# Performance work log

Hardware: AMD Instinct MI355X
Metric: run time of the kernel (lower is better)

Reference implementation:

```python
import jax, jax.numpy as jnp
import numpy as np

B, SQ, SK, D = 8, 2048, 2048, 256

def setup_inputs() -> dict:
    key = jax.random.key(0)
    ks = jax.random.split(key, 8)
    x1 = jax.random.normal(ks[0], (B, SQ, D), dtype=jnp.float32)
    x2 = jax.random.normal(ks[1], (B, SK, D), dtype=jnp.float32)
    x3 = jax.random.normal(ks[2], (B, SK, D), dtype=jnp.float32)  # unused by the original forward (value=x3 is dead)
    mask = jax.random.bernoulli(ks[3], 0.8, (B, SK))
    scale = 0.02
    Wq = jax.random.normal(ks[4], (D, D), dtype=jnp.float32) * scale
    Wk = jax.random.normal(ks[5], (D, D), dtype=jnp.float32) * scale
    Wv = jax.random.normal(ks[6], (D, D), dtype=jnp.float32) * scale
    bq = jnp.zeros((D,), jnp.float32)
    bk = jnp.zeros((D,), jnp.float32)
    bv = jnp.zeros((D,), jnp.float32)
    return {"x1": x1, "x2": x2, "x3": x3, "Wq": Wq, "Wk": Wk, "Wv": Wv,
            "bq": bq, "bk": bk, "bv": bv, "mask": mask}

def reference(x1, x2, x3, Wq, Wk, Wv, bq, bk, bv, mask):
    d = x1.shape[-1]
    inv_sqrt_d = 1.0 / jnp.sqrt(jnp.asarray(d, x1.dtype))
    # Projections (single-head MHA with query scaling, as in torch MHA internals)
    q = (x1 @ Wq + bq) * inv_sqrt_d          # [B, SQ, D]
    k = x2 @ Wk + bk                          # [B, SK, D]
    v = x2 @ Wv + bv                          # forward_value(key): value projected from key input
    # Raw scores
    qk = jnp.einsum('bqd,bkd->bqk', q, k)     # [B, SQ, SK]
    # Mask-derived per-column rescale: qk /= (mask.size(0)/mask.sum(-2))**0.5
    m = mask.astype(qk.dtype)                 # [B, SK]
    col_count = jnp.sum(m, axis=0, keepdims=True)           # [1, SK]
    factor = jnp.sqrt(jnp.asarray(mask.shape[0], qk.dtype) / col_count)  # [1, SK]
    qk = qk / factor                          # broadcast over [B, SQ, SK]; div-by-inf -> 0 where column count is 0
    attn = jax.nn.softmax(qk, axis=-1)
    # dropout is identity in eval / p=0
    out = jnp.einsum('bqk,bkd->bqd', attn, v)  # [B, SQ, D]
    return out
```

## Files before the change

### kernel.cpp

```cpp
#include <hip/hip_runtime.h>
#include <hip/hip_bf16.h>
#include <math.h>

#define B_  8
#define SQ_ 2048
#define SK_ 2048
#define D_  256
#define NSPLIT 4
#define KEYS_PER_SPLIT (SK_ / NSPLIT)
#define NT (KEYS_PER_SPLIT / 32)

typedef __attribute__((ext_vector_type(8))) short bf16x8;
typedef __attribute__((ext_vector_type(4))) float f32x4;
typedef __attribute__((ext_vector_type(4))) unsigned short u16x4;
typedef __attribute__((ext_vector_type(8))) _Float16 f16x8;
typedef __attribute__((ext_vector_type(4))) _Float16 f16x4;
typedef __attribute__((ext_vector_type(4))) unsigned int u32x4;

static __device__ __forceinline__ unsigned short f2bf(float f) {
    unsigned int u = __builtin_bit_cast(unsigned int, f);
    u += 0x7FFFu + ((u >> 16) & 1u);
    return (unsigned short)(u >> 16);
}

static __device__ __forceinline__ void gld_lds16(const unsigned short* g, unsigned short* l) {
    __builtin_amdgcn_global_load_lds(
        (const __attribute__((address_space(1))) unsigned int*)g,
        (__attribute__((address_space(3))) unsigned int*)l, 16, 0, 0);
}

__global__ void prep_kernel(const float* __restrict__ Wq, const float* __restrict__ Wk,
                            const float* __restrict__ Wv, const int* __restrict__ mask,
                            unsigned short* __restrict__ wP, float* __restrict__ r) {
    int bid = blockIdx.x, tid = threadIdx.x;
    if (bid < 96) {
        int p = bid >> 5, c = (bid >> 2) & 7, it = bid & 3;
        const float* W = (p == 0 ? Wq : (p == 1 ? Wk : Wv));
        int chunk = it * 256 + tid;
        int nt = chunk >> 6, lane = chunk & 63;
        int l15 = lane & 15, quad = lane >> 4;
        int n = nt * 16 + l15;
        unsigned short* dst = wP + (size_t)(((p * 8 + c) * 16 + nt) * 1024 + lane * 8);
#pragma unroll
        for (int j = 0; j < 8; j++)
            dst[j] = f2bf(W[(size_t)(c * 32 + quad * 8 + j) * D_ + n]);
    } else {
        int s = (bid - 96) * 256 + tid;
        float c = 0.f;
#pragma unroll
        for (int b = 0; b < B_; b++) c += (mask[b * SK_ + s] != 0) ? 1.f : 0.f;
        r[s] = sqrtf(c * 0.125f);
    }
}

__global__ __launch_bounds__(256) void proj_kernel(
    const float* __restrict__ x1, const float* __restrict__ x2,
    const float* __restrict__ bq, const float* __restrict__ bk, const float* __restrict__ bv,
    const unsigned short* __restrict__ wP, const float* __restrict__ r,
    unsigned short* __restrict__ qb, unsigned short* __restrict__ kP,
    unsigned short* __restrict__ vP)
{
    __shared__ unsigned short sbuf[18432];
    const int tid = threadIdx.x;
    const int wv = tid >> 6, lane = tid & 63, l15 = lane & 15, quad = lane >> 4;
    const int mt = blockIdx.x, b = blockIdx.y, p = blockIdx.z;
    const int s0w = mt * 64 + wv * 16;

    const float* x = (p == 0 ? x1 : x2) + ((size_t)b * SQ_ + s0w + l15) * D_;
    const unsigned short* wbase = wP + (size_t)(p * 8) * 16 * 1024;
    const float* bias = (p == 0 ? bq : (p == 1 ? bk : bv));

    float4 xa[8], xb[8];
#pragma unroll
    for (int c = 0; c < 8; c++) {
        xa[c] = *(const float4*)(x + c * 32 + quad * 8);
        xb[c] = *(const float4*)(x + c * 32 + quad * 8 + 4);
    }
    bf16x8 af[8];
#pragma unroll
    for (int c = 0; c < 8; c++) {
        bf16x8 t;
        t[0] = (short)f2bf(xa[c].x); t[1] = (short)f2bf(xa[c].y);
        t[2] = (short)f2bf(xa[c].z); t[3] = (short)f2bf(xa[c].w);
        t[4] = (short)f2bf(xb[c].x); t[5] = (short)f2bf(xb[c].y);
        t[6] = (short)f2bf(xb[c].z); t[7] = (short)f2bf(xb[c].w);
        af[c] = t;
    }

    float bb[16];
#pragma unroll
    for (int nt = 0; nt < 16; nt++) bb[nt] = bias[nt * 16 + l15];

    f32x4 acc[16];
#pragma unroll
    for (int n = 0; n < 16; n++) acc[n] = (f32x4){0.f, 0.f, 0.f, 0.f};

#pragma unroll
    for (int c = 0; c < 8; c++) {
        const unsigned short* wc = wbase + (size_t)c * 16 * 1024 + lane * 8;
#pragma unroll
        for (int nt = 0; nt < 16; nt++) {
            bf16x8 wf = *(const bf16x8*)(wc + nt * 1024);
            acc[nt] = __builtin_amdgcn_mfma_f32_16x16x32_bf16(af[c], wf, acc[nt], 0, 0, 0);
        }
    }

    if (p == 2) {
#pragma unroll
        for (int nt = 0; nt < 16; nt++) {
            int d = nt * 16 + l15;
            u16x4 u;
#pragma unroll
            for (int g = 0; g < 4; g++) u[g] = f2bf(acc[nt][g] + bb[nt]);
            *(u16x4*)(sbuf + (size_t)d * 72 + wv * 16 + quad * 4) = u;
        }
        __syncthreads();
#pragma unroll
        for (int it = 0; it < 8; it++) {
            int chunk = it * 256 + tid;
            int tt = chunk >> 10, n = (chunk >> 6) & 15, ln = chunk & 63;
            bf16x8 v = *(const bf16x8*)(sbuf + (size_t)(n * 16 + (ln & 15)) * 72 + tt * 32 + (ln >> 4) * 8);
            *(bf16x8*)(vP + (((size_t)(b * 64 + mt * 2 + tt) * 16 + n) * 512) + ln * 8) = v;
        }
    } else if (p == 0) {
        float rv = 0.0625f;
        unsigned short* my = sbuf + wv * 2176;
#pragma unroll
        for (int h = 0; h < 2; h++) {
#pragma unroll
            for (int nt8 = 0; nt8 < 8; nt8++) {
                int nt = h * 8 + nt8;
#pragma unroll
                for (int g = 0; g < 4; g++) {
                    float v = (acc[nt][g] + bb[nt]) * rv;
                    my[(quad * 4 + g) * 136 + nt8 * 16 + l15] = f2bf(v);
                }
            }
            asm volatile("s_waitcnt lgkmcnt(0)" ::: "memory");
#pragma unroll
            for (int i2 = 0; i2 < 4; i2++) {
                int row = i2 * 4 + quad;
                bf16x8 v = *(const bf16x8*)(my + row * 136 + l15 * 8);
                *(bf16x8*)(qb + ((size_t)(b * SQ_ + s0w + row)) * D_ + h * 128 + l15 * 8) = v;
            }
        }
    } else {
        const int t = mt * 2 + (wv >> 1), hfrag = wv & 1;
        float rv[4];
#pragma unroll
        for (int g = 0; g < 4; g++) rv[g] = r[s0w + quad * 4 + g];
        unsigned short* my = sbuf + wv * 2176;
#pragma unroll
        for (int hp = 0; hp < 2; hp++) {
#pragma unroll
            for (int nt8 = 0; nt8 < 8; nt8++) {
                int nt = hp * 8 + nt8;
#pragma unroll
                for (int g = 0; g < 4; g++) {
                    float v = (acc[nt][g] + bb[nt]) * rv[g];
                    my[(quad * 4 + g) * 136 + nt8 * 16 + l15] = f2bf(v);
                }
            }
            asm volatile("s_waitcnt lgkmcnt(0)" ::: "memory");
#pragma unroll
            for (int cc = 0; cc < 4; cc++) {
                bf16x8 v = *(const bf16x8*)(my + (size_t)l15 * 136 + cc * 32 + quad * 8);
                *(bf16x8*)(kP + ((((size_t)(b * 64 + t) * 2 + hfrag) * 8 + hp * 4 + cc) * 512) + lane * 8) = v;
            }
        }
    }
}

__global__ __launch_bounds__(256, 2) void flash_kernel(
    const unsigned short* __restrict__ qb, const unsigned short* __restrict__ kP,
    const unsigned short* __restrict__ vP, _Float16* __restrict__ Op,
    float* __restrict__ lp)
{
    __shared__ unsigned short Ks[2][16 * 512];
    __shared__ unsigned short Vs[2][16 * 512];
    const int tid = threadIdx.x;
    const int wv = tid >> 6, lane = tid & 63, l15 = lane & 15, quad = lane >> 4;
    const int bid = blockIdx.x;
    const int g = bid & 31, q = bid >> 5;
    const int b = g >> 2, sp = g & 3;
    const int q0 = q * 128 + wv * 32;

    const unsigned short* kpb = kP + (size_t)(b * 64 + sp * 16) * 8192;
    const unsigned short* vpb = vP + (size_t)(b * 64 + sp * 16) * 8192;

    const int c0 = tid * 8;

#pragma unroll
    for (int i = 0; i < 4; i++)
        gld_lds16(kpb + (size_t)i * 2048 + c0, &Ks[0][i * 2048 + wv * 512]);
#pragma unroll
    for (int i = 0; i < 4; i++)
        gld_lds16(vpb + (size_t)i * 2048 + c0, &Vs[0][i * 2048 + wv * 512]);

    bf16x8 qf[2][8];
#pragma unroll
    for (int mt = 0; mt < 2; mt++) {
        const unsigned short* qrow = qb + ((size_t)(b * SQ_ + q0 + mt * 16 + l15)) * D_;
#pragma unroll
        for (int c = 0; c < 8; c++)
            qf[mt][c] = *(const bf16x8*)(qrow + c * 32 + quad * 8);
    }

    f32x4 o[2][16];
#pragma unroll
    for (int mt = 0; mt < 2; mt++)
#pragma unroll
        for (int n = 0; n < 16; n++) o[mt][n] = (f32x4){0.f, 0.f, 0.f, 0.f};
    float l_[2] = {0.f, 0.f};

    const unsigned short* kfr = &Ks[0][0] + lane * 8;
    const unsigned short* vfr = &Vs[0][0] + lane * 8;

    for (int kt = 0; kt < NT; kt++) {
        const int cur = kt & 1;
        __syncthreads();
        if (kt + 1 < NT) {
            const unsigned short* kn = kpb + (size_t)(kt + 1) * 8192;
            const unsigned short* vn = vpb + (size_t)(kt + 1) * 8192;
#pragma unroll
            for (int i = 0; i < 4; i++)
                gld_lds16(kn + (size_t)i * 2048 + c0, &Ks[cur ^ 1][i * 2048 + wv * 512]);
#pragma unroll
            for (int i = 0; i < 4; i++)
                gld_lds16(vn + (size_t)i * 2048 + c0, &Vs[cur ^ 1][i * 2048 + wv * 512]);
        }
        const unsigned short* kc = kfr + cur * (16 * 512);
        const unsigned short* vc = vfr + cur * (16 * 512);

        f32x4 s[2][2];
        s[0][0] = (f32x4){0.f,0.f,0.f,0.f}; s[0][1] = (f32x4){0.f,0.f,0.f,0.f};
        s[1][0] = (f32x4){0.f,0.f,0.f,0.f}; s[1][1] = (f32x4){0.f,0.f,0.f,0.f};
        __builtin_amdgcn_s_setprio(1);
#pragma unroll
        for (int h = 0; h < 2; h++)
#pragma unroll
            for (int c = 0; c < 8; c++) {
                bf16x8 kf = *(const bf16x8*)(kc + (h * 8 + c) * 512);
                s[0][h] = __builtin_amdgcn_mfma_f32_16x16x32_bf16(kf, qf[0][c], s[0][h], 0, 0, 0);
                s[1][h] = __builtin_amdgcn_mfma_f32_16x16x32_bf16(kf, qf[1][c], s[1][h], 0, 0, 0);
            }
        __builtin_amdgcn_s_setprio(0);

        bf16x8 pf[2];
#pragma unroll
        for (int mt = 0; mt < 2; mt++) {
            float e0 = __expf(s[mt][0][0]), e1 = __expf(s[mt][0][1]);
            float e2 = __expf(s[mt][0][2]), e3 = __expf(s[mt][0][3]);
            float f0 = __expf(s[mt][1][0]), f1 = __expf(s[mt][1][1]);
            float f2 = __expf(s[mt][1][2]), f3 = __expf(s[mt][1][3]);
            l_[mt] += (e0 + e1 + e2 + e3) + (f0 + f1 + f2 + f3);
            unsigned int pk0, pk1, pk2, pk3;
            asm("v_cvt_pk_bf16_f32 %0, %1, %2" : "=v"(pk0) : "v"(e0), "v"(e1));
            asm("v_cvt_pk_bf16_f32 %0, %1, %2" : "=v"(pk1) : "v"(e2), "v"(e3));
            asm("v_cvt_pk_bf16_f32 %0, %1, %2" : "=v"(pk2) : "v"(f0), "v"(f1));
            asm("v_cvt_pk_bf16_f32 %0, %1, %2" : "=v"(pk3) : "v"(f2), "v"(f3));
            asm("v_permlane32_swap_b32 %0, %1" : "+v"(pk0), "+v"(pk2));
            asm("v_permlane16_swap_b32 %0, %1" : "+v"(pk0), "+v"(pk2));
            asm("v_permlane32_swap_b32 %0, %1" : "+v"(pk1), "+v"(pk3));
            asm("v_permlane16_swap_b32 %0, %1" : "+v"(pk1), "+v"(pk3));
            u32x4 w = (u32x4){pk0, pk1, pk2, pk3};
            pf[mt] = __builtin_bit_cast(bf16x8, w);
        }

        __builtin_amdgcn_s_setprio(1);
#pragma unroll
        for (int n = 0; n < 16; n++) {
            bf16x8 vf = *(const bf16x8*)(vc + n * 512);
            o[0][n] = __builtin_amdgcn_mfma_f32_16x16x32_bf16(vf, pf[0], o[0][n], 0, 0, 0);
            o[1][n] = __builtin_amdgcn_mfma_f32_16x16x32_bf16(vf, pf[1], o[1][n], 0, 0, 0);
        }
        __builtin_amdgcn_s_setprio(0);
    }

#pragma unroll
    for (int mt = 0; mt < 2; mt++) {
        float t = l_[mt];
        t += __shfl_xor(t, 16, 64);
        t += __shfl_xor(t, 32, 64);
        l_[mt] = t;
    }

    _Float16* op = Op + ((size_t)(sp * B_ + b) * SQ_ + q0) * D_;
#pragma unroll
    for (int mt = 0; mt < 2; mt++) {
        _Float16* rowp = op + (size_t)(mt * 16 + l15) * D_ + quad * 4;
#pragma unroll
        for (int n = 0; n < 16; n++) {
            f16x4 v4;
#pragma unroll
            for (int g2 = 0; g2 < 4; g2++) v4[g2] = (_Float16)(o[mt][n][g2]);
            *(f16x4*)(rowp + n * 16) = v4;
        }
    }
    if (quad == 0) {
        float* lpp = lp + (size_t)(sp * B_ + b) * SQ_ + q0;
        lpp[l15] = l_[0];
        lpp[16 + l15] = l_[1];
    }
}

__global__ __launch_bounds__(256) void combine_kernel(
    const _Float16* __restrict__ Op, const float* __restrict__ lp,
    float* __restrict__ out)
{
    const int gid = blockIdx.x * 256 + threadIdx.x;
    const int row = gid >> 5;
    const size_t base = (size_t)gid * 8;
    float l = lp[row] + lp[B_ * SQ_ + row] + lp[2 * B_ * SQ_ + row] + lp[3 * B_ * SQ_ + row];
    float inv = 1.f / l;
    float acc[8] = {0,0,0,0,0,0,0,0};
#pragma unroll
    for (int sp = 0; sp < NSPLIT; sp++) {
        f16x8 v = *(const f16x8*)(Op + (size_t)sp * B_ * SQ_ * D_ + base);
#pragma unroll
        for (int j = 0; j < 8; j++) acc[j] += (float)v[j];
    }
    float4 r0 = {acc[0] * inv, acc[1] * inv, acc[2] * inv, acc[3] * inv};
    float4 r1 = {acc[4] * inv, acc[5] * inv, acc[6] * inv, acc[7] * inv};
    *(float4*)(out + base) = r0;
    *(float4*)(out + base + 4) = r1;
}

extern "C" void kernel_launch(void* const* d_in, const int* in_sizes, int n_in,
                              void* d_out, int out_size, void* d_ws, size_t ws_size,
                              hipStream_t stream)
{
    const float* x1 = (const float*)d_in[0];
    const float* x2 = (const float*)d_in[1];
    const float* Wq = (const float*)d_in[3];
    const float* Wk = (const float*)d_in[4];
    const float* Wv = (const float*)d_in[5];
    const float* bq = (const float*)d_in[6];
    const float* bk = (const float*)d_in[7];
    const float* bv = (const float*)d_in[8];
    const int*  mask = (const int*)d_in[9];
    float* out = (float*)d_out;

    char* ws = (char*)d_ws;
    unsigned short* qb = (unsigned short*)(ws);
    unsigned short* kP = (unsigned short*)(ws + 8388608);
    unsigned short* vP = (unsigned short*)(ws + 16777216);
    float*          r  = (float*)(ws + 25165824);
    float*          lp = (float*)(ws + 25174016);
    _Float16*       Op = (_Float16*)(ws + 25436160);
    unsigned short* wP = (unsigned short*)(ws + 25436160);

    prep_kernel<<<dim3(96 + SK_ / 256), 256, 0, stream>>>(Wq, Wk, Wv, mask, wP, r);
    proj_kernel<<<dim3(SQ_ / 64, B_, 3), 256, 0, stream>>>(x1, x2, bq, bk, bv, wP, r, qb, kP, vP);
    flash_kernel<<<dim3((SQ_ / 128) * B_ * NSPLIT), 256, 0, stream>>>(qb, kP, vP, Op, lp);
    combine_kernel<<<dim3((B_ * SQ_ * D_ / 8) / 256), 256, 0, stream>>>(Op, lp, out);
}
```

Before: 175.6 us.

## Stage K/V LDS reads into register batches with split barriers and explicit vmcnt waits

Restructures the attention inner loop into four phases (two K halves, two V halves). Each phase batches its LDS fragment reads into registers, issues the async global-to-LDS prefetch for the next tile in parts (K during the first QK half, V during the second), and synchronises with raw s_barrier plus explicit vmcnt/lgkmcnt waits instead of a full __syncthreads. The aim is to overlap LDS reads and global prefetch with MFMA work and shorten barrier stalls. In exchange the hand-tuned waitcnt values must match the number of outstanding loads exactly, the kernel now has four barriers per tile instead of one, and the extra fragment registers raise register pressure.

```diff
diff --git a/kernel.cpp b/kernel.cpp
--- a/kernel.cpp
+++ b/kernel.cpp
@@ -28,6 +28,10 @@
         (const __attribute__((address_space(1))) unsigned int*)g,
         (__attribute__((address_space(3))) unsigned int*)l, 16, 0, 0);
 }
+
+#define VMCNT(n)  asm volatile("s_waitcnt vmcnt(" #n ")" ::: "memory")
+#define LGKM0_SB  do { asm volatile("s_waitcnt lgkmcnt(0)" ::: "memory"); \
+                       __builtin_amdgcn_sched_barrier(0); } while (0)
 
 __global__ void prep_kernel(const float* __restrict__ Wq, const float* __restrict__ Wk,
                             const float* __restrict__ Wv, const int* __restrict__ mask,
@@ -218,32 +222,50 @@
 
     for (int kt = 0; kt < NT; kt++) {
         const int cur = kt & 1;
-        __syncthreads();
-        if (kt + 1 < NT) {
+        const unsigned short* kc = kfr + cur * (16 * 512);
+        const unsigned short* vc = vfr + cur * (16 * 512);
+        const bool pre = (kt + 1 < NT);
+
+        VMCNT(4);
+        bf16x8 kf0[8];
+#pragma unroll
+        for (int c = 0; c < 8; c++) kf0[c] = *(const bf16x8*)(kc + c * 512);
+        if (pre) {
             const unsigned short* kn = kpb + (size_t)(kt + 1) * 8192;
-            const unsigned short* vn = vpb + (size_t)(kt + 1) * 8192;
 #pragma unroll
             for (int i = 0; i < 4; i++)
                 gld_lds16(kn + (size_t)i * 2048 + c0, &Ks[cur ^ 1][i * 2048 + wv * 512]);
-#pragma unroll
-            for (int i = 0; i < 4; i++)
-                gld_lds16(vn + (size_t)i * 2048 + c0, &Vs[cur ^ 1][i * 2048 + wv * 512]);
-        }
-        const unsigned short* kc = kfr + cur * (16 * 512);
-        const unsigned short* vc = vfr + cur * (16 * 512);
-
+        }
+        __builtin_amdgcn_s_barrier();
+        LGKM0_SB;
         f32x4 s[2][2];
         s[0][0] = (f32x4){0.f,0.f,0.f,0.f}; s[0][1] = (f32x4){0.f,0.f,0.f,0.f};
         s[1][0] = (f32x4){0.f,0.f,0.f,0.f}; s[1][1] = (f32x4){0.f,0.f,0.f,0.f};
         __builtin_amdgcn_s_setprio(1);
 #pragma unroll
-        for (int h = 0; h < 2; h++)
-#pragma unroll
-            for (int c = 0; c < 8; c++) {
-                bf16x8 kf = *(const bf16x8*)(kc + (h * 8 + c) * 512);
-                s[0][h] = __builtin_amdgcn_mfma_f32_16x16x32_bf16(kf, qf[0][c], s[0][h], 0, 0, 0);
-                s[1][h] = __builtin_amdgcn_mfma_f32_16x16x32_bf16(kf, qf[1][c], s[1][h], 0, 0, 0);
-            }
+        for (int c = 0; c < 8; c++) {
+            s[0][0] = __builtin_amdgcn_mfma_f32_16x16x32_bf16(kf0[c], qf[0][c], s[0][0], 0, 0, 0);
+            s[1][0] = __builtin_amdgcn_mfma_f32_16x16x32_bf16(kf0[c], qf[1][c], s[1][0], 0, 0, 0);
+        }
+        __builtin_amdgcn_s_setprio(0);
+
+        bf16x8 kf1[8];
+#pragma unroll
+        for (int c = 0; c < 8; c++) kf1[c] = *(const bf16x8*)(kc + (8 + c) * 512);
+        if (pre) {
+            const unsigned short* vn = vpb + (size_t)(kt + 1) * 8192;
+#pragma unroll
+            for (int i = 0; i < 4; i++)
+                gld_lds16(vn + (size_t)i * 2048 + c0, &Vs[cur ^ 1][i * 2048 + wv * 512]);
+        }
+        __builtin_amdgcn_s_barrier();
+        LGKM0_SB;
+        __builtin_amdgcn_s_setprio(1);
+#pragma unroll
+        for (int c = 0; c < 8; c++) {
+            s[0][1] = __builtin_amdgcn_mfma_f32_16x16x32_bf16(kf1[c], qf[0][c], s[0][1], 0, 0, 0);
+            s[1][1] = __builtin_amdgcn_mfma_f32_16x16x32_bf16(kf1[c], qf[1][c], s[1][1], 0, 0, 0);
+        }
         __builtin_amdgcn_s_setprio(0);
 
         bf16x8 pf[2];
@@ -267,12 +289,31 @@
             pf[mt] = __builtin_bit_cast(bf16x8, w);
         }
 
+        if (pre) { VMCNT(8); }
+        else     { VMCNT(0); }
+        bf16x8 vf0[8];
+#pragma unroll
+        for (int n = 0; n < 8; n++) vf0[n] = *(const bf16x8*)(vc + n * 512);
+        __builtin_amdgcn_s_barrier();
+        LGKM0_SB;
         __builtin_amdgcn_s_setprio(1);
 #pragma unroll
-        for (int n = 0; n < 16; n++) {
-            bf16x8 vf = *(const bf16x8*)(vc + n * 512);
-            o[0][n] = __builtin_amdgcn_mfma_f32_16x16x32_bf16(vf, pf[0], o[0][n], 0, 0, 0);
-            o[1][n] = __builtin_amdgcn_mfma_f32_16x16x32_bf16(vf, pf[1], o[1][n], 0, 0, 0);
+        for (int n = 0; n < 8; n++) {
+            o[0][n] = __builtin_amdgcn_mfma_f32_16x16x32_bf16(vf0[n], pf[0], o[0][n], 0, 0, 0);
+            o[1][n] = __builtin_amdgcn_mfma_f32_16x16x32_bf16(vf0[n], pf[1], o[1][n], 0, 0, 0);
+        }
+        __builtin_amdgcn_s_setprio(0);
+
+        bf16x8 vf1[8];
+#pragma unroll
+        for (int n = 0; n < 8; n++) vf1[n] = *(const bf16x8*)(vc + (8 + n) * 512);
+        __builtin_amdgcn_s_barrier();
+        LGKM0_SB;
+        __builtin_amdgcn_s_setprio(1);
+#pragma unroll
+        for (int n = 0; n < 8; n++) {
+            o[0][8 + n] = __builtin_amdgcn_mfma_f32_16x16x32_bf16(vf1[n], pf[0], o[0][8 + n], 0, 0, 0);
+            o[1][8 + n] = __builtin_amdgcn_mfma_f32_16x16x32_bf16(vf1[n], pf[1], o[1][8 + n], 0, 0, 0);
         }
         __builtin_amdgcn_s_setprio(0);
     }
```

After: 178.4 us. About the same (+1.6%).
